# Optimization experiments

Hardware: AMD Instinct MI355X
Metric: run time of the kernel (lower is better)

Reference implementation:

```python
import jax, jax.numpy as jnp
import numpy as np
from jax.scipy.sparse.linalg import cg

SCALE = 8      # scaling_factor
CROP = 256     # crop_size
FEAT = 32      # per-branch feature channels
CG_ITERS = 100


def _conv(x, w, b):
    y = jax.lax.conv_general_dilated(x, w, (1, 1), 'SAME',
                                     dimension_numbers=('NCHW', 'OIHW', 'NCHW'))
    return y + b[None, :, None, None]


def _avgpool(x, r):
    B, C, H, W = x.shape
    return x.reshape(B, C, H // r, r, W // r, r).mean(axis=(3, 5))


def _up_adj(x, r):
    # adjoint of average-pool downsampling S: spread value / r^2 over the block
    return jnp.repeat(jnp.repeat(x, r, axis=2), r, axis=3) / (r * r)


def _features(guide, y_bicubic, gw1, gb1, gw2, gb2, sw1, sb1, sw2, sb2):
    g = _conv(jax.nn.relu(_conv(guide, gw1, gb1)), gw2, gb2)
    s = _conv(jax.nn.relu(_conv(y_bicubic, sw1, sb1)), sw2, sb2)
    return jnp.concatenate([g, s], axis=1)  # [B, 2*FEAT, H, W]


def _neighbor_affinity(f, mu, lam):
    # exp(-mu * ||f_i - f_j||^2) to the 4 grid neighbors, zero affinity at borders
    dv = jnp.sum((f[:, :, 1:, :] - f[:, :, :-1, :]) ** 2, axis=1)  # [B,H-1,W]
    dh = jnp.sum((f[:, :, :, 1:] - f[:, :, :, :-1]) ** 2, axis=1)  # [B,H,W-1]
    wv = jnp.exp(-mu * dv)
    wh = jnp.exp(-mu * dh)
    w_up = jnp.pad(wv, ((0, 0), (1, 0), (0, 0)))
    w_dn = jnp.pad(wv, ((0, 0), (0, 1), (0, 0)))
    w_lf = jnp.pad(wh, ((0, 0), (0, 0), (1, 0)))
    w_rt = jnp.pad(wh, ((0, 0), (0, 0), (0, 1)))
    deg = w_up + w_dn + w_lf + w_rt
    center = deg + lam  # diagonal of the system matrix (channel 4)
    return jnp.stack([w_up, w_dn, w_lf, w_rt, center], axis=1)  # [B,5,H,W]


def _graph_matvec(aff, mask_lr, lam, y):
    # A y = (D - W) y + lam * S^T M S y   (5-point graph Laplacian + LR data term)
    w_up, w_dn, w_lf, w_rt, center = (aff[:, i] for i in range(5))
    yy = y[:, 0]
    wy = (w_up * jnp.pad(yy[:, :-1, :], ((0, 0), (1, 0), (0, 0)))
          + w_dn * jnp.pad(yy[:, 1:, :], ((0, 0), (0, 1), (0, 0)))
          + w_lf * jnp.pad(yy[:, :, :-1], ((0, 0), (0, 0), (1, 0)))
          + w_rt * jnp.pad(yy[:, :, 1:], ((0, 0), (0, 0), (0, 1))))
    deg = center - lam
    lap = (deg * yy - wy)[:, None]
    data = lam * _up_adj(mask_lr * _avgpool(y, SCALE), SCALE)
    return lap + data


def setup_inputs() -> dict:
    key = jax.random.key(0)
    ks = jax.random.split(key, 20)
    B, H = 16, CROP
    r = SCALE
    w = lambda k, sh: jax.random.normal(k, sh, jnp.float32) * 0.05
    return {
        'guide': jax.random.normal(ks[0], (B, 3, H, H), jnp.float32),
        'source': jax.random.normal(ks[1], (B, 1, H // r, H // r), jnp.float32),
        'mask_lr': jnp.ones((B, 1, H // r, H // r), jnp.float32),
        'y_bicubic': jax.random.normal(ks[2], (B, 1, H, H), jnp.float32),
        # feature extractor (guide branch + source branch)
        'gw1': w(ks[3], (FEAT, 3, 3, 3)), 'gb1': jnp.zeros((FEAT,), jnp.float32),
        'gw2': w(ks[4], (FEAT, FEAT, 3, 3)), 'gb2': jnp.zeros((FEAT,), jnp.float32),
        'sw1': w(ks[5], (FEAT, 1, 3, 3)), 'sb1': jnp.zeros((FEAT,), jnp.float32),
        'sw2': w(ks[6], (FEAT, FEAT, 3, 3)), 'sb2': jnp.zeros((FEAT,), jnp.float32),
        # var_conv: VarEstimateModule(in=4, out=1, k=3)
        'vw1': w(ks[7], (FEAT, 4, 3, 3)), 'vb1': jnp.zeros((FEAT,), jnp.float32),
        'vw2': w(ks[8], (FEAT, FEAT, 3, 3)), 'vb2': jnp.zeros((FEAT,), jnp.float32),
        'vw3': w(ks[9], (1, FEAT, 3, 3)), 'vb3': jnp.zeros((1,), jnp.float32),
        # learned scalars (stored as log, as in the torch module)
        'log_lambda': jnp.log(jnp.array([1.0], jnp.float32)),
        'log_mu': jnp.log(jnp.array([0.1], jnp.float32)),
    }


def reference(guide, source, mask_lr, y_bicubic,
              gw1, gb1, gw2, gb2, sw1, sb1, sw2, sb2,
              vw1, vb1, vw2, vb2, vw3, vb3,
              log_lambda, log_mu):
    mu = jnp.exp(log_mu)[0]
    lam = jnp.exp(log_lambda)[0]
    # variance head on cat([guide, y_bicubic])
    v = jnp.concatenate([guide, y_bicubic], axis=1)
    v = jax.nn.relu(_conv(v, vw1, vb1))
    v = jax.nn.relu(_conv(v, vw2, vb2))
    var = _conv(v, vw3, vb3)
    # pixel affinities from multi-modal features
    feats = _features(guide, y_bicubic, gw1, gb1, gw2, gb2, sw1, sb1, sw2, sb2)
    aff = _neighbor_affinity(feats, mu, lam)
    # graph-regularised SR: solve (L + lam S^T M S) y = lam S^T (M source) by CG
    b = lam * _up_adj(mask_lr * source, SCALE)
    matvec = lambda y: _graph_matvec(aff, mask_lr, lam, y)
    y_pred, _ = cg(matvec, b, x0=y_bicubic, maxiter=CG_ITERS, tol=1e-6)
    return y_pred, var, aff
```

## Files before the change

### kernel.cpp

```cpp
#include <hip/hip_runtime.h>
#include <hip/hip_bf16.h>

typedef __hip_bfloat16 bf16;
typedef __attribute__((ext_vector_type(8))) short short8;
typedef __attribute__((ext_vector_type(4))) float f32x4;

#define NB 16
#define PLANE (256*256)

static __device__ __forceinline__ short f2bf(float v){
    __hip_bfloat16 h = __float2bfloat16(v);
    short s; __builtin_memcpy(&s, &h, 2); return s;
}
static __device__ __forceinline__ float bf2f(short s){
    union { unsigned u; float f; } cv;
    cv.u = ((unsigned)(unsigned short)s) << 16; return cv.f;
}

static __device__ __forceinline__ void  stg_ag(float* p, float v){
    __hip_atomic_store(p, v, __ATOMIC_RELAXED, __HIP_MEMORY_SCOPE_AGENT);
}
static __device__ __forceinline__ float ldg_ag(const float* p){
    return __hip_atomic_load(p, __ATOMIC_RELAXED, __HIP_MEMORY_SCOPE_AGENT);
}
static __device__ __forceinline__ void stg4_ag(float* p, f32x4 v){
    asm volatile("global_store_dwordx4 %0, %1, off sc0 sc1" :: "v"(p), "v"(v) : "memory");
}
static __device__ __forceinline__ f32x4 ldg4_ag(const float* p){
    f32x4 r;
    asm volatile("global_load_dwordx4 %0, %1, off sc0 sc1\n\ts_waitcnt vmcnt(0)"
                 : "=v"(r) : "v"(p) : "memory");
    return r;
}

template<int CIN, int SPLIT>
static __device__ __forceinline__ void conv1_body(
    const float* __restrict__ in, const float* __restrict__ in2,
    const float* __restrict__ wgt, const float* __restrict__ bias,
    bf16* __restrict__ out, float* s_in, float* s_w,
    int n, int ty0, int tx0, int tid)
{
    for (int idx = tid; idx < CIN*9*32; idx += 256) {
        int co = idx & 31; int rest = idx >> 5;
        s_w[idx] = wgt[(co*CIN + rest/9)*9 + rest%9];
    }
    for (int idx = tid; idx < CIN*18*18; idx += 256) {
        int ci = idx / 324; int rr = idx % 324;
        int yy = rr / 18, xx = rr % 18;
        int y = ty0 + yy - 1, x = tx0 + xx - 1;
        float v = 0.f;
        if (y >= 0 && y < 256 && x >= 0 && x < 256) {
            if (ci < SPLIT) v = in [((size_t)(n*SPLIT + ci)*256 + y)*256 + x];
            else            v = in2[((size_t)(n*(CIN-SPLIT) + (ci-SPLIT))*256 + y)*256 + x];
        }
        s_in[ci*324 + yy*18 + xx] = v;
    }
    __syncthreads();

    const int ty = tid >> 4, tx = tid & 15;
    float acc[32];
    #pragma unroll
    for (int co = 0; co < 32; co++) acc[co] = bias[co];

    #pragma unroll
    for (int ci = 0; ci < CIN; ci++) {
        #pragma unroll
        for (int ky = 0; ky < 3; ky++)
        #pragma unroll
        for (int kx = 0; kx < 3; kx++) {
            float v = s_in[ci*324 + (ty+ky)*18 + (tx+kx)];
            const float* wp = &s_w[(ci*9 + ky*3 + kx)*32];
            #pragma unroll
            for (int co = 0; co < 32; co++) acc[co] = fmaf(v, wp[co], acc[co]);
        }
    }
    const int y = ty0 + ty, x = tx0 + tx;
    size_t base = (((size_t)n*256 + y)*256 + x)*32;
    #pragma unroll
    for (int c = 0; c < 32; c += 8) {
        short8 vv;
        #pragma unroll
        for (int j = 0; j < 8; j++)
            vv[j] = f2bf(fmaxf(acc[c+j], 0.f));
        *(short8*)((short*)out + base + c) = vv;
    }
}

__global__ __launch_bounds__(256)
void conv1_gs(const float* __restrict__ guide, const float* __restrict__ ybic,
              const float* __restrict__ gw1, const float* __restrict__ gb1,
              const float* __restrict__ sw1, const float* __restrict__ sb1,
              bf16* __restrict__ outg, bf16* __restrict__ outs)
{
    __shared__ float s_in[3*324];
    __shared__ float s_w[3*9*32];
    const int zz = blockIdx.z;
    const int br = zz >> 4, n = zz & 15;
    const int ty0 = blockIdx.y * 16, tx0 = blockIdx.x * 16;
    if (br == 0)
        conv1_body<3,3>(guide, guide, gw1, gb1, outg, s_in, s_w, n, ty0, tx0, threadIdx.x);
    else
        conv1_body<1,1>(ybic, ybic, sw1, sb1, outs, s_in, s_w, n, ty0, tx0, threadIdx.x);
}

__global__ __launch_bounds__(256)
void wrepack3(const float* __restrict__ a, const float* __restrict__ b,
              const float* __restrict__ c,
              bf16* __restrict__ oa, bf16* __restrict__ ob, bf16* __restrict__ oc)
{
    int j = blockIdx.x*256 + threadIdx.x;
    if (j >= 3*9216) return;
    int set = j / 9216, r = j % 9216;
    int tap = r >> 10, rem = r & 1023, co = rem >> 5, ci = rem & 31;
    const float* src = (set == 0) ? a : (set == 1) ? b : c;
    bf16* dst = (set == 0) ? oa : (set == 1) ? ob : oc;
    dst[r] = __float2bfloat16(src[(co*32 + ci)*9 + tap]);
}

template<bool RELU>
__global__ __launch_bounds__(256)
void conv3x3_mfma(const bf16* __restrict__ in, const bf16* __restrict__ wpk,
                  const float* __restrict__ bias, bf16* __restrict__ out)
{
    __shared__ __align__(16) short s_a[4*2640];
    const int tid = threadIdx.x;
    const int lane = tid & 63, wid = tid >> 6;
    const int m = lane & 15, quad = lane >> 4, k0 = quad*8;
    const int n  = blockIdx.z;
    const int x0 = blockIdx.x * 16;
    const int y0 = blockIdx.y * 16;

    const short* inp = (const short*)in + (size_t)n*PLANE*32;
    short* outp = (short*)out + (size_t)n*PLANE*32;

    for (int c = tid; c < 1296; c += 256) {
        int q = c & 3, px = c >> 2;
        int yy = px / 18, xx = px - yy*18;
        int gy = y0 + yy - 1, gx = x0 + xx - 1;
        short8 v = {0,0,0,0,0,0,0,0};
        if ((unsigned)gy < 256u && (unsigned)gx < 256u)
            v = *(const short8*)(inp + ((size_t)(gy*256 + gx))*32 + q*8);
        *(short8*)(s_a + q*2640 + (yy*18 + xx)*8) = v;
    }

    const short* wp = (const short*)wpk;
    short8 bw[2][9];
    #pragma unroll
    for (int g = 0; g < 2; g++)
        #pragma unroll
        for (int tap = 0; tap < 9; tap++)
            bw[g][tap] = *(const short8*)(wp + ((tap*32 + g*16 + m)*32 + k0));
    const float b0 = bias[m], b1 = bias[16 + m];
    __syncthreads();

    const short* sa = s_a + quad*2640;
    #pragma unroll
    for (int r = 0; r < 4; r++) {
        const int lr = wid*4 + r;
        f32x4 acc0 = { b0, b0, b0, b0 };
        f32x4 acc1 = { b1, b1, b1, b1 };
        #pragma unroll
        for (int ky = 0; ky < 3; ky++)
        #pragma unroll
        for (int kx = 0; kx < 3; kx++) {
            short8 a = *(const short8*)(sa + ((lr+ky)*18 + (m+kx))*8);
            acc0 = __builtin_amdgcn_mfma_f32_16x16x32_bf16(a, bw[0][ky*3+kx], acc0, 0, 0, 0);
            acc1 = __builtin_amdgcn_mfma_f32_16x16x32_bf16(a, bw[1][ky*3+kx], acc1, 0, 0, 0);
        }
        const int y = y0 + lr;
        #pragma unroll
        for (int reg = 0; reg < 4; reg++) {
            int px = x0 + quad*4 + reg;
            size_t idx = ((size_t)y*256 + px)*32;
            float v0 = acc0[reg], v1 = acc1[reg];
            if (RELU) { v0 = fmaxf(v0, 0.f); v1 = fmaxf(v1, 0.f); }
            outp[idx + m]      = f2bf(v0);
            outp[idx + 16 + m] = f2bf(v1);
        }
    }
}

__global__ __launch_bounds__(256, 2)
void conv2gs_dvdh(const bf16* __restrict__ ing, const bf16* __restrict__ ins,
                  const bf16* __restrict__ wpk1, const float* __restrict__ gb2,
                  const bf16* __restrict__ wpk2, const float* __restrict__ sb2,
                  float* __restrict__ dv, float* __restrict__ dh)
{
    __shared__ __align__(16) short s_a[4*2896];
    __shared__ __align__(16) short s_f[17*17*40];
    const int tid = threadIdx.x;
    const int lane = tid & 63, wid = tid >> 6;
    const int m = lane & 15, quad = lane >> 4, k0 = quad*8;
    const int zz = blockIdx.z;
    const int br = zz >> 4, n = zz & 15;
    const int x0 = blockIdx.x * 16;
    const int y0 = blockIdx.y * 16;

    const bf16* in = br ? ins : ing;
    const bf16* wpk = br ? wpk2 : wpk1;
    const float* bias = br ? sb2 : gb2;

    const short* inp = (const short*)in + (size_t)n*PLANE*32;

    for (int c = tid; c < 1444; c += 256) {
        int q = c & 3, px = c >> 2;
        int yy = px / 19, xx = px - yy*19;
        int gy = y0 + yy - 1, gx = x0 + xx - 1;
        short8 v = {0,0,0,0,0,0,0,0};
        if ((unsigned)gy < 256u && (unsigned)gx < 256u)
            v = *(const short8*)(inp + ((size_t)(gy*256 + gx))*32 + q*8);
        *(short8*)(s_a + q*2896 + (yy*19 + xx)*8) = v;
    }

    const short* wp = (const short*)wpk;
    short8 bw[2][9];
    #pragma unroll
    for (int g = 0; g < 2; g++)
        #pragma unroll
        for (int tap = 0; tap < 9; tap++)
            bw[g][tap] = *(const short8*)(wp + ((tap*32 + g*16 + m)*32 + k0));
    const float b0 = bias[m], b1 = bias[16 + m];
    __syncthreads();

    const short* sa = s_a + quad*2896;

    for (int ru = 0; ru < 5; ru++) {
        const int yl = wid + 4*ru;
        if (yl > 16) break;
        f32x4 acc0 = { b0, b0, b0, b0 };
        f32x4 acc1 = { b1, b1, b1, b1 };
        #pragma unroll
        for (int ky = 0; ky < 3; ky++)
        #pragma unroll
        for (int kx = 0; kx < 3; kx++) {
            short8 a = *(const short8*)(sa + ((yl+ky)*19 + (kx+m))*8);
            acc0 = __builtin_amdgcn_mfma_f32_16x16x32_bf16(a, bw[0][ky*3+kx], acc0, 0, 0, 0);
            acc1 = __builtin_amdgcn_mfma_f32_16x16x32_bf16(a, bw[1][ky*3+kx], acc1, 0, 0, 0);
        }
        #pragma unroll
        for (int reg = 0; reg < 4; reg++) {
            int c = quad*4 + reg;
            short* fp = s_f + (yl*17 + c)*40;
            fp[m]      = f2bf(acc0[reg]);
            fp[16 + m] = f2bf(acc1[reg]);
        }
    }

    for (int ru = 0; ru < 4; ru++) {
        const int yl = wid + 4*ru;
        f32x4 acc0 = { b0, b0, b0, b0 };
        f32x4 acc1 = { b1, b1, b1, b1 };
        #pragma unroll
        for (int ky = 0; ky < 3; ky++)
        #pragma unroll
        for (int kx = 0; kx < 3; kx++) {
            int col = 16 + kx + m; if (col > 18) col = 18;
            short8 a = *(const short8*)(sa + ((yl+ky)*19 + col)*8);
            acc0 = __builtin_amdgcn_mfma_f32_16x16x32_bf16(a, bw[0][ky*3+kx], acc0, 0, 0, 0);
            acc1 = __builtin_amdgcn_mfma_f32_16x16x32_bf16(a, bw[1][ky*3+kx], acc1, 0, 0, 0);
        }
        if (quad == 0) {
            short* fp = s_f + (yl*17 + 16)*40;
            fp[m]      = f2bf(acc0[0]);
            fp[16 + m] = f2bf(acc1[0]);
        }
    }
    __syncthreads();

    const int ty = tid >> 4, tx = tid & 15;
    const int i = y0 + ty, j = x0 + tx;
    const short8* pc = (const short8*)(s_f + (ty*17 + tx)*40);
    const short8* pr = (j < 255) ? (const short8*)(s_f + (ty*17 + tx + 1)*40) : pc;
    const short8* pd = (i < 255) ? (const short8*)(s_f + ((ty+1)*17 + tx)*40) : pc;
    float adv = 0.f, adh = 0.f;
    #pragma unroll
    for (int c4 = 0; c4 < 4; c4++) {
        short8 sc = pc[c4], sr = pr[c4], sd = pd[c4];
        #pragma unroll
        for (int e = 0; e < 8; e++) {
            float fc = bf2f(sc[e]);
            float d1 = bf2f(sr[e]) - fc;
            float d2 = bf2f(sd[e]) - fc;
            adh = fmaf(d1, d1, adh);
            adv = fmaf(d2, d2, adv);
        }
    }
    int o = (n*256 + i)*256 + j;
    atomicAdd(&dv[o], adv);
    atomicAdd(&dh[o], adh);
}

__global__ __launch_bounds__(256)
void conv3x3_last(const bf16* __restrict__ in, const float* __restrict__ wgt,
                  const float* __restrict__ bias, float* __restrict__ out)
{
    __shared__ float s_w[288];
    int tid = threadIdx.x;
    for (int i = tid; i < 288; i += 256) s_w[i] = wgt[i];
    __syncthreads();
    int gid = blockIdx.x*256 + tid;
    int n = gid >> 16, h = (gid >> 8) & 255, w = gid & 255;
    const short* inp = (const short*)in + (size_t)n*PLANE*32;
    float sum = bias[0];
    #pragma unroll
    for (int ky = 0; ky < 3; ky++) {
        int yy = h + ky - 1;
        if ((unsigned)yy >= 256u) continue;
        #pragma unroll
        for (int kx = 0; kx < 3; kx++) {
            int xx = w + kx - 1;
            if ((unsigned)xx >= 256u) continue;
            const short8* pp = (const short8*)(inp + ((size_t)yy*256 + xx)*32);
            int tap = ky*3 + kx;
            #pragma unroll
            for (int c4 = 0; c4 < 4; c4++) {
                short8 v = pp[c4];
                #pragma unroll
                for (int j = 0; j < 8; j++)
                    sum = fmaf(bf2f(v[j]), s_w[(c4*8+j)*9 + tap], sum);
            }
        }
    }
    out[gid] = sum;
}

__global__ __launch_bounds__(256)
void conv1v_aff(const float* __restrict__ guide, const float* __restrict__ ybic,
                const float* __restrict__ vw1, const float* __restrict__ vb1,
                bf16* __restrict__ outv,
                const float* __restrict__ dv, const float* __restrict__ dh,
                const float* __restrict__ llam, const float* __restrict__ lmu,
                unsigned* __restrict__ wvh, float* __restrict__ aff)
{
    __shared__ float s_in[4*324];
    __shared__ float s_w[4*9*32];
    const int b = blockIdx.x;
    if (b < 4096) {
        int n = b >> 8, by = (b >> 4) & 15, bx = b & 15;
        conv1_body<4,3>(guide, ybic, vw1, vb1, outv, s_in, s_w,
                        n, by*16, bx*16, threadIdx.x);
        return;
    }
    int bid = b - 4096;
    int n = bid >> 8, h = bid & 255, w = threadIdx.x;
    float mu = expf(lmu[0]), lam = expf(llam[0]);
    int rb = (n*256 + h)*256 + w;
    float wvv = (h < 255) ? expf(-mu * dv[rb]) : 0.f;
    float whv = (w < 255) ? expf(-mu * dh[rb]) : 0.f;
    unsigned pv = (unsigned)(unsigned short)f2bf(wvv);
    unsigned ph = (unsigned)(unsigned short)f2bf(whv);
    wvh[rb] = pv | (ph << 16);
    float w_up = (h > 0) ? expf(-mu * dv[rb - 256]) : 0.f;
    float w_lf = (w > 0) ? expf(-mu * dh[rb - 1])   : 0.f;
    float ctr  = w_up + wvv + w_lf + whv + lam;
    float* a = aff + ((size_t)n*5)*PLANE + h*256 + w;
    a[0]        = w_up;
    a[PLANE]    = wvv;
    a[2*PLANE]  = w_lf;
    a[3*PLANE]  = whv;
    a[4*PLANE]  = ctr;
}

__global__ __launch_bounds__(256, 2)
void cg_persist(const unsigned* __restrict__ wvh, const float* __restrict__ mask,
                const float* __restrict__ src, const float* __restrict__ ybic,
                const float* __restrict__ llam, float* __restrict__ xout,
                float* __restrict__ ebuf0, float* __restrict__ ebuf1,
                float* __restrict__ part4, float* __restrict__ res4)
{
    __shared__ float s_pn[66][34];
    __shared__ float s_part[256], s_bs[32];
    __shared__ float s_w3[12];
    __shared__ __align__(16) float s_g[16];

    const int tid = threadIdx.x;
    const int wb = blockIdx.x;
    const int n = wb >> 5, t = wb & 31;
    const int tyo = (t >> 3) * 64, txo = (t & 7) * 32;
    const int tx = tid & 31, tyb = tid >> 5;
    const int w = txo + tx;
    const float lam = expf(llam[0]);
    const bool is_leader = ((wb & 127) == 0);

    const unsigned* wn = wvh + (size_t)n*PLANE;
    const float* ybn = ybic + (size_t)n*PLANE;

    int idx[8];
    unsigned wc[8], wu[8], wl[8];
    float c1[8], rhs[8];
    #pragma unroll
    for (int i = 0; i < 8; i++) {
        int hhi = tyo + tyb + 8*i;
        idx[i] = hhi*256 + w;
        wc[i] = wn[idx[i]];
        wu[i] = (hhi > 0) ? wn[idx[i]-256] : 0u;
        wl[i] = (w > 0)   ? wn[idx[i]-1]   : 0u;
        int bi = n*1024 + (hhi>>3)*32 + (w>>3);
        float mv = mask[bi];
        c1[i]  = lam*mv*(1.f/4096.f);
        rhs[i] = lam*mv*src[bi]*(1.f/64.f);
    }

    const bool hthr = (tid < 192);
    int hy = 0, hx = 0; bool hin = false; int nb = 0, eoff = 0;
    if (hthr) {
        if      (tid < 32)  { hy = tyo - 1;         hx = txo + tid;
                              nb = wb - 8; eoff = 32 + tid; }
        else if (tid < 64)  { hy = tyo + 64;        hx = txo + (tid-32);
                              nb = wb + 8; eoff = tid - 32; }
        else if (tid < 128) { hy = tyo + (tid-64);  hx = txo - 1;
                              nb = wb - 1; eoff = 128 + (tid-64); }
        else                { hy = tyo + (tid-128); hx = txo + 32;
                              nb = wb + 1; eoff = 64 + (tid-128); }
        hin = (hy >= 0 && hy < 256 && hx >= 0 && hx < 256);
    }
    const int hsy = hy - tyo + 1, hsx = hx - txo + 1;

    #define POOL_BLOCK() do { \
        __syncthreads(); \
        { int segrow_ = tid >> 2, segcol_ = tid & 3; \
          const float* rw_ = &s_pn[1 + segrow_][1 + segcol_*8]; \
          s_part[tid] = rw_[0]+rw_[1]+rw_[2]+rw_[3]+rw_[4]+rw_[5]+rw_[6]+rw_[7]; } \
        __syncthreads(); \
        if (tid < 32) { int brow_ = tid >> 2, bcol_ = tid & 3; float s_ = 0.f; \
          _Pragma("unroll") \
          for (int rr_ = 0; rr_ < 8; rr_++) s_ += s_part[(brow_*8 + rr_)*4 + bcol_]; \
          s_bs[tid] = s_; } \
        __syncthreads(); \
    } while (0)

    #define PUBLISH_E(arr, ebase) do { \
        float* eb_ = (ebase) + (size_t)wb*192; \
        if (tyb == 0) stg_ag(eb_ + tx, arr[0]); \
        if (tyb == 7) stg_ag(eb_ + 32 + tx, arr[7]); \
        if (tx == 0) { _Pragma("unroll") \
            for (int i_ = 0; i_ < 8; i_++) stg_ag(eb_ + 64 + tyb + 8*i_, arr[i_]); } \
        if (tx == 31){ _Pragma("unroll") \
            for (int i_ = 0; i_ < 8; i_++) stg_ag(eb_ + 128 + tyb + 8*i_, arr[i_]); } \
    } while (0)

    auto matvec = [&](int i) -> float {
        int yy = 1 + tyb + 8*i, xx = 1 + tx;
        float wvd = bf2f((short)(wc[i] & 0xffff));
        float whr = bf2f((short)(wc[i] >> 16));
        float wvu = bf2f((short)(wu[i] & 0xffff));
        float whl = bf2f((short)(wl[i] >> 16));
        float s = wvu*s_pn[yy-1][xx] + wvd*s_pn[yy+1][xx]
                + whl*s_pn[yy][xx-1] + whr*s_pn[yy][xx+1];
        float deg = wvu+wvd+whl+whr;
        return deg*s_pn[yy][xx] - s + c1[i]*s_bs[i*4 + (tx>>3)];
    };

    auto publish_red = [&](unsigned seq, float va, float vb, float vc){
        #pragma unroll
        for (int o = 32; o > 0; o >>= 1) {
            va += __shfl_down(va, o, 64);
            vb += __shfl_down(vb, o, 64);
            vc += __shfl_down(vc, o, 64);
        }
        asm volatile("s_waitcnt vmcnt(0)" ::: "memory");
        __syncthreads();
        if ((tid & 63) == 0) { int wv = tid >> 6; s_w3[wv*3]=va; s_w3[wv*3+1]=vb; s_w3[wv*3+2]=vc; }
        __syncthreads();
        if (tid == 0) {
            f32x4 pk;
            pk[0] = s_w3[0]+s_w3[3]+s_w3[6]+s_w3[9];
            pk[1] = s_w3[1]+s_w3[4]+s_w3[7]+s_w3[10];
            pk[2] = s_w3[2]+s_w3[5]+s_w3[8]+s_w3[11];
            pk[3] = __uint_as_float(seq);
            stg4_ag(part4 + (size_t)((seq & 1)*512 + wb)*4, pk);
        }
    };

    float o0, o1, o2;
    auto allred = [&](unsigned seq){
        float* resp = res4 + (size_t)(seq & 1)*64;
        if (is_leader && tid < 64) {
            const float* pl = part4 + (size_t)(seq & 1)*2048;
            const float* p0 = pl + (size_t)(wb + 2*tid)*4;
            f32x4 a0 = ldg4_ag(p0);
            while (__float_as_uint(a0[3]) < seq) { __builtin_amdgcn_s_sleep(1); a0 = ldg4_ag(p0); }
            f32x4 a1 = ldg4_ag(p0 + 4);
            while (__float_as_uint(a1[3]) < seq) { __builtin_amdgcn_s_sleep(1); a1 = ldg4_ag(p0 + 4); }
            float pa = a0[0] + a1[0];
            float pb = a0[1] + a1[1];
            float pc = a0[2] + a1[2];
            #pragma unroll
            for (int o = 32; o > 0; o >>= 1) {
                pa += __shfl_down(pa, o, 64);
                pb += __shfl_down(pb, o, 64);
                pc += __shfl_down(pc, o, 64);
            }
            if (tid == 0) {
                f32x4 rk; rk[0] = pa; rk[1] = pb; rk[2] = pc; rk[3] = __uint_as_float(seq);
                stg4_ag(resp + (wb >> 7)*16, rk);
            }
        }
        if (tid < 4) {
            const float* rl = resp + tid*16;
            f32x4 g = ldg4_ag(rl);
            while (__float_as_uint(g[3]) < seq) { __builtin_amdgcn_s_sleep(2); g = ldg4_ag(rl); }
            *(f32x4*)&s_g[tid*4] = g;
        }
        __syncthreads();
        o0 = ((s_g[0]+s_g[4])+s_g[8])+s_g[12];
        o1 = ((s_g[1]+s_g[5])+s_g[9])+s_g[13];
        o2 = ((s_g[2]+s_g[6])+s_g[10])+s_g[14];
    };

    float xv[8], rv[8], pv[8], apv[8];
    float rh = 0.f, phh = 0.f;

    #pragma unroll
    for (int i = 0; i < 8; i++) {
        xv[i] = ybn[idx[i]];
        s_pn[1 + tyb + 8*i][1 + tx] = xv[i];
    }
    if (hthr) s_pn[hsy][hsx] = hin ? ybn[hy*256 + hx] : 0.f;
    POOL_BLOCK();
    float g0t = 0.f;
    #pragma unroll
    for (int i = 0; i < 8; i++) {
        float ax = matvec(i);
        float r0 = rhs[i] - ax;
        rv[i] = r0; pv[i] = r0;
        g0t += r0*r0;
    }
    PUBLISH_E(pv, ebuf1);
    publish_red(1u, 0.f, 0.f, 0.f);
    allred(1u);

    {
        float hv = 0.f;
        if (hthr && hin) hv = ldg_ag(ebuf1 + (size_t)nb*192 + eoff);
        if (hthr) { rh = hv; phh = hv; s_pn[hsy][hsx] = phh; }
        #pragma unroll
        for (int i = 0; i < 8; i++) s_pn[1 + tyb + 8*i][1 + tx] = pv[i];
        POOL_BLOCK();
        float pap = 0.f, apap = 0.f;
        #pragma unroll
        for (int i = 0; i < 8; i++) {
            float ap = matvec(i);
            apv[i] = ap;
            pap  += pv[i]*ap;
            apap += ap*ap;
        }
        PUBLISH_E(apv, ebuf0);
        publish_red(2u, g0t, pap, apap);
    }

    for (int k = 1; k <= 99; k++) {
        float* ebR = ((k+1) & 1) ? ebuf1 : ebuf0;
        float* ebW = ((k+2) & 1) ? ebuf1 : ebuf0;

        allred((unsigned)(k + 1));
        float alpha = o0 / o1;
        float beta  = (alpha*alpha*o2 - o0) / o0;

        float hv = 0.f;
        if (hthr && hin) hv = ldg_ag(ebR + (size_t)nb*192 + eoff);

        float gsum = 0.f;
        #pragma unroll
        for (int i = 0; i < 8; i++) {
            float rN = fmaf(-alpha, apv[i], rv[i]);
            xv[i] = fmaf(alpha, pv[i], xv[i]);
            float pN = fmaf(beta, pv[i], rN);
            rv[i] = rN; pv[i] = pN;
            gsum += rN*rN;
            s_pn[1 + tyb + 8*i][1 + tx] = pN;
        }
        if (hthr) {
            rh  = fmaf(-alpha, hv, rh);
            phh = fmaf(beta, phh, rh);
            s_pn[hsy][hsx] = phh;
        }
        POOL_BLOCK();
        float pap = 0.f, apap = 0.f;
        #pragma unroll
        for (int i = 0; i < 8; i++) {
            float ap = matvec(i);
            apv[i] = ap;
            pap  += pv[i]*ap;
            apap += ap*ap;
        }
        PUBLISH_E(apv, ebW);
        publish_red((unsigned)(k + 2), gsum, pap, apap);
    }

    allred(101u);
    float alphaT = o0 / o1;
    float* xn = xout + (size_t)n*PLANE;
    #pragma unroll
    for (int i = 0; i < 8; i++) xn[idx[i]] = fmaf(alphaT, pv[i], xv[i]);

    #undef POOL_BLOCK
    #undef PUBLISH_E
}

extern "C" void kernel_launch(void* const* d_in, const int* in_sizes, int n_in,
                              void* d_out, int out_size, void* d_ws, size_t ws_size,
                              hipStream_t stream)
{
    (void)in_sizes; (void)n_in; (void)out_size; (void)ws_size;
    const float* guide = (const float*)d_in[0];
    const float* source= (const float*)d_in[1];
    const float* mask  = (const float*)d_in[2];
    const float* ybic  = (const float*)d_in[3];
    const float* gw1 = (const float*)d_in[4];  const float* gb1 = (const float*)d_in[5];
    const float* gw2 = (const float*)d_in[6];  const float* gb2 = (const float*)d_in[7];
    const float* sw1 = (const float*)d_in[8];  const float* sb1 = (const float*)d_in[9];
    const float* sw2 = (const float*)d_in[10]; const float* sb2 = (const float*)d_in[11];
    const float* vw1 = (const float*)d_in[12]; const float* vb1 = (const float*)d_in[13];
    const float* vw2 = (const float*)d_in[14]; const float* vb2 = (const float*)d_in[15];
    const float* vw3 = (const float*)d_in[16]; const float* vb3 = (const float*)d_in[17];
    const float* llam = (const float*)d_in[18];
    const float* lmu  = (const float*)d_in[19];

    float* out     = (float*)d_out;
    float* x_out   = out;
    float* var_out = out + 1048576;
    float* aff_out = out + 2097152;

    char* ws = (char*)d_ws;
    float*    res4  = (float*)ws;
    float*    part4 = (float*)(ws + 4096);
    bf16*     wpk1  = (bf16*)(ws + 24576);
    bf16*     wpk2  = (bf16*)(ws + 43008);
    bf16*     wpk3  = (bf16*)(ws + 61440);
    unsigned* wvh   = (unsigned*)(ws + 131072);
    char*     A     = ws + 131072 + (size_t)NB*PLANE*4;
    bf16*  tmpA = (bf16*)(A);
    bf16*  tmpB = (bf16*)(A + (size_t)NB*32*PLANE*2);
    float* dv   = (float*)(A + (size_t)NB*32*PLANE*4);
    float* dh   = (float*)(A + (size_t)NB*32*PLANE*4 + (size_t)NB*PLANE*4);
    float* ebuf0 = (float*)A;
    float* ebuf1 = (float*)(A + (size_t)512*192*4);

    hipMemsetAsync(ws, 0, 20480, stream);
    hipMemsetAsync(dv, 0, (size_t)2*NB*PLANE*4, stream);

    wrepack3<<<108,256,0,stream>>>(gw2, sw2, vw2, wpk1, wpk2, wpk3);

    conv1_gs<<<dim3(16,16,2*NB),256,0,stream>>>(guide, ybic, gw1, gb1, sw1, sb1,
                                                tmpA, tmpB);
    conv2gs_dvdh<<<dim3(16,16,2*NB),256,0,stream>>>(tmpA, tmpB, wpk1, gb2, wpk2, sb2,
                                                    dv, dh);
    conv1v_aff<<<8192,256,0,stream>>>(guide, ybic, vw1, vb1, tmpA,
                                      dv, dh, llam, lmu, wvh, aff_out);
    conv3x3_mfma<true><<<dim3(16,16,NB),256,0,stream>>>(tmpA, wpk3, vb2, tmpB);
    conv3x3_last<<<4096,256,0,stream>>>(tmpB, vw3, vb3, var_out);

    cg_persist<<<512,256,0,stream>>>(wvh, mask, source, ybic, llam, x_out,
                                     ebuf0, ebuf1, part4, res4);
}
```

Before: 876.0 us.

## Fuse variance-head second conv and final conv via shared-memory halo recompute

Merges the MFMA 3x3 conv (32->32, ReLU) and the final 32->1 conv of the variance head into one kernel. Each block loads a 20x20 input tile and computes an 18x18 intermediate tile in LDS, recomputing the halo. The last conv then reads LDS instead of global memory. This removes the global round trip of the 32-channel bf16 intermediate and one launch, at the cost of redundant MFMA work for the halo rows and columns and more LDS per block.

```diff
diff --git a/kernel.cpp b/kernel.cpp
--- a/kernel.cpp
+++ b/kernel.cpp
@@ -117,69 +117,6 @@
     dst[r] = __float2bfloat16(src[(co*32 + ci)*9 + tap]);
 }
 
-template<bool RELU>
-__global__ __launch_bounds__(256)
-void conv3x3_mfma(const bf16* __restrict__ in, const bf16* __restrict__ wpk,
-                  const float* __restrict__ bias, bf16* __restrict__ out)
-{
-    __shared__ __align__(16) short s_a[4*2640];
-    const int tid = threadIdx.x;
-    const int lane = tid & 63, wid = tid >> 6;
-    const int m = lane & 15, quad = lane >> 4, k0 = quad*8;
-    const int n  = blockIdx.z;
-    const int x0 = blockIdx.x * 16;
-    const int y0 = blockIdx.y * 16;
-
-    const short* inp = (const short*)in + (size_t)n*PLANE*32;
-    short* outp = (short*)out + (size_t)n*PLANE*32;
-
-    for (int c = tid; c < 1296; c += 256) {
-        int q = c & 3, px = c >> 2;
-        int yy = px / 18, xx = px - yy*18;
-        int gy = y0 + yy - 1, gx = x0 + xx - 1;
-        short8 v = {0,0,0,0,0,0,0,0};
-        if ((unsigned)gy < 256u && (unsigned)gx < 256u)
-            v = *(const short8*)(inp + ((size_t)(gy*256 + gx))*32 + q*8);
-        *(short8*)(s_a + q*2640 + (yy*18 + xx)*8) = v;
-    }
-
-    const short* wp = (const short*)wpk;
-    short8 bw[2][9];
-    #pragma unroll
-    for (int g = 0; g < 2; g++)
-        #pragma unroll
-        for (int tap = 0; tap < 9; tap++)
-            bw[g][tap] = *(const short8*)(wp + ((tap*32 + g*16 + m)*32 + k0));
-    const float b0 = bias[m], b1 = bias[16 + m];
-    __syncthreads();
-
-    const short* sa = s_a + quad*2640;
-    #pragma unroll
-    for (int r = 0; r < 4; r++) {
-        const int lr = wid*4 + r;
-        f32x4 acc0 = { b0, b0, b0, b0 };
-        f32x4 acc1 = { b1, b1, b1, b1 };
-        #pragma unroll
-        for (int ky = 0; ky < 3; ky++)
-        #pragma unroll
-        for (int kx = 0; kx < 3; kx++) {
-            short8 a = *(const short8*)(sa + ((lr+ky)*18 + (m+kx))*8);
-            acc0 = __builtin_amdgcn_mfma_f32_16x16x32_bf16(a, bw[0][ky*3+kx], acc0, 0, 0, 0);
-            acc1 = __builtin_amdgcn_mfma_f32_16x16x32_bf16(a, bw[1][ky*3+kx], acc1, 0, 0, 0);
-        }
-        const int y = y0 + lr;
-        #pragma unroll
-        for (int reg = 0; reg < 4; reg++) {
-            int px = x0 + quad*4 + reg;
-            size_t idx = ((size_t)y*256 + px)*32;
-            float v0 = acc0[reg], v1 = acc1[reg];
-            if (RELU) { v0 = fmaxf(v0, 0.f); v1 = fmaxf(v1, 0.f); }
-            outp[idx + m]      = f2bf(v0);
-            outp[idx + 16 + m] = f2bf(v1);
-        }
-    }
-}
-
 __global__ __launch_bounds__(256, 2)
 void conv2gs_dvdh(const bf16* __restrict__ ing, const bf16* __restrict__ ins,
                   const bf16* __restrict__ wpk1, const float* __restrict__ gb2,
@@ -290,18 +227,89 @@
     atomicAdd(&dh[o], adh);
 }
 
-__global__ __launch_bounds__(256)
-void conv3x3_last(const bf16* __restrict__ in, const float* __restrict__ wgt,
-                  const float* __restrict__ bias, float* __restrict__ out)
-{
-    __shared__ float s_w[288];
-    int tid = threadIdx.x;
-    for (int i = tid; i < 288; i += 256) s_w[i] = wgt[i];
+__global__ __launch_bounds__(256, 2)
+void conv2v_last(const bf16* __restrict__ in, const bf16* __restrict__ wpk,
+                 const float* __restrict__ bias,
+                 const float* __restrict__ vw3, const float* __restrict__ vb3,
+                 float* __restrict__ var_out)
+{
+    __shared__ __align__(16) short s_a[4*3248];
+    __shared__ __align__(16) short s_f[18*18*40];
+    __shared__ float s_w3[288];
+    const int tid = threadIdx.x;
+    const int lane = tid & 63, wid = tid >> 6;
+    const int m = lane & 15, quad = lane >> 4, k0 = quad*8;
+    const int n  = blockIdx.z;
+    const int x0 = blockIdx.x * 16;
+    const int y0 = blockIdx.y * 16;
+
+    const short* inp = (const short*)in + (size_t)n*PLANE*32;
+
+    for (int c = tid; c < 1600; c += 256) {
+        int q = c & 3, px = c >> 2;
+        int yy = px / 20, xx = px - yy*20;
+        int gy = y0 + yy - 2, gx = x0 + xx - 2;
+        short8 v = {0,0,0,0,0,0,0,0};
+        if ((unsigned)gy < 256u && (unsigned)gx < 256u)
+            v = *(const short8*)(inp + ((size_t)(gy*256 + gx))*32 + q*8);
+        *(short8*)(s_a + q*3248 + (yy*20 + xx)*8) = v;
+    }
+    for (int i = tid; i < 288; i += 256) s_w3[i] = vw3[i];
+
+    const short* wp = (const short*)wpk;
+    short8 bw[2][9];
+    #pragma unroll
+    for (int g = 0; g < 2; g++)
+        #pragma unroll
+        for (int tap = 0; tap < 9; tap++)
+            bw[g][tap] = *(const short8*)(wp + ((tap*32 + g*16 + m)*32 + k0));
+    const float b0 = bias[m], b1 = bias[16 + m];
     __syncthreads();
-    int gid = blockIdx.x*256 + tid;
-    int n = gid >> 16, h = (gid >> 8) & 255, w = gid & 255;
-    const short* inp = (const short*)in + (size_t)n*PLANE*32;
-    float sum = bias[0];
+
+    const short* sa = s_a + quad*3248;
+    for (int ly = wid; ly < 18; ly += 4) {
+        f32x4 acc0 = { b0, b0, b0, b0 };
+        f32x4 acc1 = { b1, b1, b1, b1 };
+        #pragma unroll
+        for (int ky = 0; ky < 3; ky++)
+        #pragma unroll
+        for (int kx = 0; kx < 3; kx++) {
+            short8 a = *(const short8*)(sa + ((ly+ky)*20 + (m+kx))*8);
+            acc0 = __builtin_amdgcn_mfma_f32_16x16x32_bf16(a, bw[0][ky*3+kx], acc0, 0, 0, 0);
+            acc1 = __builtin_amdgcn_mfma_f32_16x16x32_bf16(a, bw[1][ky*3+kx], acc1, 0, 0, 0);
+        }
+        #pragma unroll
+        for (int reg = 0; reg < 4; reg++) {
+            int lx = quad*4 + reg;
+            short* fp = s_f + (ly*18 + lx)*40;
+            fp[m]      = f2bf(fmaxf(acc0[reg], 0.f));
+            fp[16 + m] = f2bf(fmaxf(acc1[reg], 0.f));
+        }
+        f32x4 e0 = { b0, b0, b0, b0 };
+        f32x4 e1 = { b1, b1, b1, b1 };
+        #pragma unroll
+        for (int ky = 0; ky < 3; ky++)
+        #pragma unroll
+        for (int kx = 0; kx < 3; kx++) {
+            int col = 16 + m + kx; if (col > 19) col = 19;
+            short8 a = *(const short8*)(sa + ((ly+ky)*20 + col)*8);
+            e0 = __builtin_amdgcn_mfma_f32_16x16x32_bf16(a, bw[0][ky*3+kx], e0, 0, 0, 0);
+            e1 = __builtin_amdgcn_mfma_f32_16x16x32_bf16(a, bw[1][ky*3+kx], e1, 0, 0, 0);
+        }
+        if (quad == 0) {
+            #pragma unroll
+            for (int reg = 0; reg < 2; reg++) {
+                short* fp = s_f + (ly*18 + 16 + reg)*40;
+                fp[m]      = f2bf(fmaxf(e0[reg], 0.f));
+                fp[16 + m] = f2bf(fmaxf(e1[reg], 0.f));
+            }
+        }
+    }
+    __syncthreads();
+
+    const int ty = tid >> 4, tx = tid & 15;
+    const int h = y0 + ty, w = x0 + tx;
+    float sum = vb3[0];
     #pragma unroll
     for (int ky = 0; ky < 3; ky++) {
         int yy = h + ky - 1;
@@ -310,18 +318,18 @@
         for (int kx = 0; kx < 3; kx++) {
             int xx = w + kx - 1;
             if ((unsigned)xx >= 256u) continue;
-            const short8* pp = (const short8*)(inp + ((size_t)yy*256 + xx)*32);
+            const short8* pp = (const short8*)(s_f + ((ty+ky)*18 + (tx+kx))*40);
             int tap = ky*3 + kx;
             #pragma unroll
             for (int c4 = 0; c4 < 4; c4++) {
                 short8 v = pp[c4];
                 #pragma unroll
                 for (int j = 0; j < 8; j++)
-                    sum = fmaf(bf2f(v[j]), s_w[(c4*8+j)*9 + tap], sum);
+                    sum = fmaf(bf2f(v[j]), s_w3[(c4*8+j)*9 + tap], sum);
             }
         }
     }
-    out[gid] = sum;
+    var_out[(size_t)n*PLANE + h*256 + w] = sum;
 }
 
 __global__ __launch_bounds__(256)
@@ -648,8 +656,7 @@
                                                     dv, dh);
     conv1v_aff<<<8192,256,0,stream>>>(guide, ybic, vw1, vb1, tmpA,
                                       dv, dh, llam, lmu, wvh, aff_out);
-    conv3x3_mfma<true><<<dim3(16,16,NB),256,0,stream>>>(tmpA, wpk3, vb2, tmpB);
-    conv3x3_last<<<4096,256,0,stream>>>(tmpB, vw3, vb3, var_out);
+    conv2v_last<<<dim3(16,16,NB),256,0,stream>>>(tmpA, wpk3, vb2, vw3, vb3, var_out);
 
     cg_persist<<<512,256,0,stream>>>(wvh, mask, source, ybic, llam, x_out,
                                      ebuf0, ebuf1, part4, res4);
```

Measured after the change: 868.2 us. About the same (-0.9%).
